# Kernel optimization log

Measured on AMD Instinct MI355X. Metric: run time of the kernel, lower is better.

The kernel has to match this reference:

```python
import jax, jax.numpy as jnp
import numpy as np

B, Tc, E, K, M, V = 8, 1024, 256, 8, 2048, 16
T1 = Tc * K          # penultimate layer length = 8192
TLAST = M * K        # last layer length = 16384


def setup_inputs() -> dict:
    key = jax.random.key(0)
    ks = jax.random.split(key, 12)
    x = jax.random.normal(ks[0], (B, Tc, E), jnp.float32)
    # penultimate values: exactly M 'mixed' tokens (value==2) per row, rest in {1,3}
    base = jnp.where(jnp.arange(T1) < M, 2, 1 + 2 * jax.random.randint(ks[1], (B, T1), 0, 2))
    perm = jnp.argsort(jax.random.uniform(ks[2], (B, T1)), axis=1)
    val1 = jnp.take_along_axis(base, perm, axis=1)
    vallast = 1 + 2 * jax.random.randint(ks[3], (B, TLAST), 0, 2)
    value = jnp.concatenate([val1, vallast], axis=1).astype(jnp.int64)
    depth = jnp.concatenate([jnp.full((B, T1), 5), jnp.full((B, TLAST), 6)], axis=1).astype(jnp.int64)
    pos = jax.random.randint(ks[4], (B, T1 + TLAST, 3), 0, 64).astype(jnp.int64)
    s = 0.02
    W1 = s * jax.random.normal(ks[5], (E, E, K), jnp.float32)  # ConvTranspose1d weight [in,out,k]
    b1 = s * jax.random.normal(ks[6], (E,), jnp.float32)
    W0 = s * jax.random.normal(ks[7], (E, E, K), jnp.float32)
    b0 = s * jax.random.normal(ks[8], (E,), jnp.float32)
    Wl = s * jax.random.normal(ks[9], (V + 1, E), jnp.float32)
    bl = s * jax.random.normal(ks[10], (V + 1,), jnp.float32)
    return {"x": x, "value": value, "depth": depth, "pos": pos, "num_mix": M,
            "W1": W1, "b1": b1, "W0": W0, "b0": b0, "Wl": Wl, "bl": bl}


def _deconv(x, W, b):
    # ConvTranspose1d with kernel=stride=K: each token expands to K tokens
    n, t, e = x.shape
    o = W.shape[1]
    y = jnp.einsum('nte,eoj->ntjo', x, W)  # [N,T,K,O]
    return y.reshape(n, t * W.shape[2], o) + b


def reference(x, value, depth, pos, num_mix, W1, b1, W0, b0, Wl, bl):
    n, tc, e = x.shape
    k = W1.shape[2]
    t1 = tc * k
    max_depth = jnp.max(depth)
    len_1 = jnp.sum(depth == max_depth - 1, axis=1)               # [N]
    tt = jnp.arange(t1)
    val_1 = jnp.where(tt[None, :] < len_1[:, None], value[:, :t1], 0)  # padded penultimate values
    mix_mask = val_1 == 2                                         # [N,T1]
    mix_1 = jnp.sum(mix_mask, axis=1)                             # [N]
    y_1 = _deconv(x, W1, b1)                                      # [N,T1,E]
    # stable pack: bring positions with value==2 to the front, keep order
    order = jnp.argsort(jnp.where(mix_mask, 0, 1), axis=1, stable=True)
    sel = order[:, :num_mix]                                      # [N,M]
    x_0 = jnp.take_along_axis(y_1, sel[:, :, None], axis=1)       # [N,M,E]
    valid = (jnp.arange(num_mix)[None, :] < mix_1[:, None]).astype(x_0.dtype)
    x_0 = x_0 * valid[:, :, None]                                 # zero-pad beyond per-row mix count
    y_0 = _deconv(x_0, W0, b0)                                    # [N,M*K,E]
    return y_0 @ Wl.T + bl                                        # [N,M*K,V+1]
```

## Files before the change

### kernel.cpp

```cpp
#include <hip/hip_runtime.h>

typedef __attribute__((ext_vector_type(8))) short bf16x8;
typedef __attribute__((ext_vector_type(4))) float f32x4;

#define BB 8
#define TC 1024
#define EE 256
#define KJ 8
#define MSEL 2048
#define V1 17
#define T1 8192
#define TTOT 24576
#define BI_TOT 16384
#define NCOLP 160
#define WSTRIDE 264

#define SCAL_OFF 0
#define SEL_OFF  1024
#define GRP_OFF  (SEL_OFF + 65536)
#define WFT_OFF  (GRP_OFF + 524288)
#define B2_OFF   (WFT_OFF + NCOLP*WSTRIDE*2)
#define BF0_OFF  (B2_OFF + 640)
#define WCT_OFF  (BF0_OFF + 128)

__device__ __forceinline__ unsigned short f2bf(float f) {
    union { float f; unsigned u; } x; x.f = f;
    unsigned r = x.u + 0x7fffu + ((x.u >> 16) & 1u);
    return (unsigned short)(r >> 16);
}
__device__ __forceinline__ float bf2f(unsigned short h) {
    union { unsigned u; float f; } x; x.u = ((unsigned)h) << 16;
    return x.f;
}

__device__ __forceinline__ float blockReduceSum256(float v) {
    #pragma unroll
    for (int d = 32; d; d >>= 1) v += __shfl_down(v, d, 64);
    __shared__ float sm[4];
    int lane = threadIdx.x & 63, wid = threadIdx.x >> 6;
    if (lane == 0) sm[wid] = v;
    __syncthreads();
    return sm[0] + sm[1] + sm[2] + sm[3];
}

__global__ __launch_bounds__(256) void k_maxdepth(const int* depth, int* scal) {
    int idx = blockIdx.x * 256 + threadIdx.x;
    int4 d = ((const int4*)depth)[idx];
    int v = max(max(d.x, d.y), max(d.z, d.w));
    #pragma unroll
    for (int dd = 32; dd; dd >>= 1) v = max(v, __shfl_down(v, dd, 64));
    __shared__ int sm[4];
    int lane = threadIdx.x & 63, wid = threadIdx.x >> 6;
    if (lane == 0) sm[wid] = v;
    __syncthreads();
    if (threadIdx.x == 0) atomicMax(&scal[0], max(max(sm[0], sm[1]), max(sm[2], sm[3])));
    if (blockIdx.x == 0 && threadIdx.x < 31) scal[1 + threadIdx.x] = 0;
}

__global__ __launch_bounds__(256) void k_len1(const int* depth, int* scal) {
    int idx = blockIdx.x * 256 + threadIdx.x;
    int b = blockIdx.x / 24;
    int md1 = scal[0] - 1;
    int4 d = ((const int4*)depth)[idx];
    int c = (d.x == md1) + (d.y == md1) + (d.z == md1) + (d.w == md1);
    #pragma unroll
    for (int dd = 32; dd; dd >>= 1) c += __shfl_down(c, dd, 64);
    __shared__ int sm[4];
    int lane = threadIdx.x & 63, wid = threadIdx.x >> 6;
    if (lane == 0) sm[wid] = c;
    __syncthreads();
    if (threadIdx.x == 0) {
        int t = sm[0] + sm[1] + sm[2] + sm[3];
        if (t) atomicAdd(&scal[1 + b], t);
    }
}

__global__ __launch_bounds__(256) void k_scan(const int* value, int* scal, int* sel) {
    int b = blockIdx.x, tid = threadIdx.x;
    int len1 = scal[1 + b];
    const int* vb = value + b * TTOT;
    int t0 = tid * 32;
    unsigned mask = 0;
    #pragma unroll
    for (int k = 0; k < 32; k += 4) {
        int4 v = *(const int4*)(vb + t0 + k);
        if (t0 + k + 0 < len1 && v.x == 2) mask |= 1u << (k + 0);
        if (t0 + k + 1 < len1 && v.y == 2) mask |= 1u << (k + 1);
        if (t0 + k + 2 < len1 && v.z == 2) mask |= 1u << (k + 2);
        if (t0 + k + 3 < len1 && v.w == 2) mask |= 1u << (k + 3);
    }
    int cnt = __popc(mask);
    int inc = cnt;
    #pragma unroll
    for (int d = 1; d < 64; d <<= 1) {
        int n = __shfl_up(inc, d, 64);
        if ((tid & 63) >= d) inc += n;
    }
    __shared__ int wt[4];
    int lane = tid & 63, wid = tid >> 6;
    if (lane == 63) wt[wid] = inc;
    __syncthreads();
    int woff = 0;
    for (int w = 0; w < wid; ++w) woff += wt[w];
    int off = woff + inc - cnt;
    #pragma unroll
    for (int k = 0; k < 32; ++k) {
        if (mask & (1u << k)) {
            if (off < MSEL) sel[b * MSEL + off] = t0 + k;
            off++;
        }
    }
    if (tid == 0) scal[9 + b] = wt[0] + wt[1] + wt[2] + wt[3];
}

__global__ __launch_bounds__(256) void k_wfused(const float* W0, const float* Wl, unsigned short* wfT) {
    int em = blockIdx.x;
    __shared__ float w0s[EE * KJ];
    __shared__ float wls[V1 * 257];
    for (int idx = threadIdx.x; idx < EE * KJ; idx += 256) w0s[idx] = W0[em * EE * KJ + idx];
    for (int idx = threadIdx.x; idx < V1 * EE; idx += 256) {
        int v = idx >> 8, o = idx & 255;
        wls[v * 257 + o] = Wl[idx];
    }
    __syncthreads();
    int tid = threadIdx.x;
    if (tid < 136) {
        int j = tid / V1, v = tid - j * V1;
        float acc = 0.f;
        #pragma unroll 4
        for (int o = 0; o < EE; ++o) acc += w0s[o * KJ + j] * wls[v * 257 + o];
        wfT[(j * 20 + v) * WSTRIDE + em] = f2bf(acc);
    }
}

__global__ __launch_bounds__(256) void k_grpbias(const int* sel, int* scal, int* groups,
        const float* b0, const float* bl, const float* b1, const float* Wl,
        const unsigned short* wfT, float* bias2, float* bf0) {
    int bid = blockIdx.x, tid = threadIdx.x;
    if (bid < 64) {
        __shared__ int lcnt[KJ], lbase[KJ];
        if (tid < KJ) lcnt[tid] = 0;
        __syncthreads();
        int idx = bid * 256 + tid;
        int b = idx >> 11;
        int valid = ((idx & (MSEL - 1)) < scal[9 + b]) ? 1 : 0;
        int t = valid ? sel[idx] : 0;
        int g = t & 7, tq = t >> 3;
        int lslot = atomicAdd(&lcnt[g], 1);
        __syncthreads();
        if (tid < KJ) lbase[tid] = atomicAdd(&scal[17 + tid], lcnt[tid]);
        __syncthreads();
        groups[g * BI_TOT + lbase[g] + lslot] = (idx << 11) | (tq << 1) | valid;
    } else if (bid < 81) {
        int v = bid - 64;
        float s = blockReduceSum256(b0[tid] * Wl[v * EE + tid]);
        if (tid == 0) bf0[v] = s + bl[v];
    } else {
        int c17 = bid - 81;
        int j = c17 / V1, v = c17 - j * V1;
        int colP = j * 20 + v;
        float s = blockReduceSum256(b1[tid] * bf2f(wfT[colP * WSTRIDE + tid]));
        if (tid == 0) bias2[colP] = s;
    }
}

__global__ __launch_bounds__(256) void k_wcomb(const float* W1, const unsigned short* wfT,
                                               unsigned short* wct) {
    int g = blockIdx.x >> 3;
    int e0 = (blockIdx.x & 7) * 32;
    __shared__ __align__(16) unsigned short b1s[32 * WSTRIDE];
    __shared__ __align__(16) unsigned short af[NCOLP * 72];
    int tid = threadIdx.x;
    {
        int em_l = tid & 63;
        int eb = (tid >> 6) * 8;
        #pragma unroll
        for (int i = 0; i < 8; ++i) {
            int e = eb + i;
            #pragma unroll
            for (int c = 0; c < 4; ++c) {
                int em = c * 64 + em_l;
                b1s[e * WSTRIDE + em] = f2bf(W1[(e0 + e) * (EE * KJ) + em * KJ + g]);
            }
        }
    }
    for (int idx = tid; idx < 1280; idx += 256) {
        int row = idx >> 3, f = idx & 7;
        ((int4*)af)[row * 9 + f] = ((const int4*)wfT)[row * 33 + f];
    }
    __syncthreads();

    int w = tid >> 6, l = tid & 63;
    int ntile = w & 1, mhalf = w >> 1;
    int lr = l & 15, lq = l >> 4;
    f32x4 acc[5];
    #pragma unroll
    for (int t = 0; t < 5; ++t) acc[t] = (f32x4){0.f, 0.f, 0.f, 0.f};

    for (int ch = 0; ch < 4; ++ch) {
        if (ch) {
            __syncthreads();
            for (int idx = tid; idx < 1280; idx += 256) {
                int row = idx >> 3, f = idx & 7;
                ((int4*)af)[row * 9 + f] = ((const int4*)wfT)[row * 33 + ch * 8 + f];
            }
            __syncthreads();
        }
        #pragma unroll
        for (int s = 0; s < 2; ++s) {
            bf16x8 bfr = *(const bf16x8*)&b1s[(ntile * 16 + lr) * WSTRIDE + ch * 64 + s * 32 + lq * 8];
            #pragma unroll
            for (int t = 0; t < 5; ++t) {
                bf16x8 afr = *(const bf16x8*)&af[((mhalf * 5 + t) * 16 + lr) * 72 + s * 32 + lq * 8];
                acc[t] = __builtin_amdgcn_mfma_f32_16x16x32_bf16(afr, bfr, acc[t], 0, 0, 0);
            }
        }
    }
    #pragma unroll
    for (int t = 0; t < 5; ++t) {
        int m = (mhalf * 5 + t) * 16 + lq * 4;
        int n = e0 + ntile * 16 + lr;
        #pragma unroll
        for (int r = 0; r < 4; ++r)
            wct[(g * NCOLP + m + r) * WSTRIDE + n] = f2bf(acc[t][r]);
    }
}

__global__ __launch_bounds__(256) void k_main(const float* x, const unsigned short* wct,
        const int* scal, const int* groups, const float* bias2, const float* bf0, float* out) {
    int g = blockIdx.x >> 9;
    int tile = blockIdx.x & 511;
    int cntg = scal[17 + g];
    if (tile * 32 >= cntg) return;
    int nrows = min(32, cntg - tile * 32);

    __shared__ __align__(16) unsigned short xs[32 * WSTRIDE];
    __shared__ __align__(16) unsigned short wts[NCOLP * 72];
    __shared__ int xoffs[32], obase[32];
    __shared__ unsigned char vflag[32];

    int tid = threadIdx.x;
    if (tid < 32) {
        int flag = 0, xo = 0, ob = 0;
        if (tid < nrows) {
            int p = groups[g * BI_TOT + tile * 32 + tid];
            int valid = p & 1;
            int tq = (p >> 1) & 1023;
            int bi = p >> 11;
            int b = bi >> 11;
            xo = (b * TC + tq) * EE;
            ob = bi * 136;
            flag = 1 + valid;
        }
        xoffs[tid] = xo; obase[tid] = ob; vflag[tid] = (unsigned char)flag;
    }
    __syncthreads();
    {
        int row = tid >> 3, q = tid & 7;
        const float* xp = x + xoffs[row];
        #pragma unroll
        for (int i = 0; i < 8; ++i) {
            int f4 = q + 8 * i;
            float4 v = *(const float4*)(xp + f4 * 4);
            ushort4 pk;
            pk.x = f2bf(v.x); pk.y = f2bf(v.y); pk.z = f2bf(v.z); pk.w = f2bf(v.w);
            *(ushort4*)&xs[row * WSTRIDE + f4 * 4] = pk;
        }
    }
    const int4* wsrc = (const int4*)wct;
    for (int idx = tid; idx < 1280; idx += 256) {
        int row = idx >> 3, f = idx & 7;
        ((int4*)wts)[row * 9 + f] = wsrc[(g * NCOLP + row) * 33 + f];
    }
    __syncthreads();

    int w = tid >> 6, l = tid & 63;
    int rw = w & 1, chalf = w >> 1;
    int lr = l & 15, lq = l >> 4;
    f32x4 acc[5];
    #pragma unroll
    for (int t = 0; t < 5; ++t) acc[t] = (f32x4){0.f, 0.f, 0.f, 0.f};

    for (int ch = 0; ch < 4; ++ch) {
        if (ch) {
            __syncthreads();
            for (int idx = tid; idx < 1280; idx += 256) {
                int row = idx >> 3, f = idx & 7;
                ((int4*)wts)[row * 9 + f] = wsrc[(g * NCOLP + row) * 33 + ch * 8 + f];
            }
            __syncthreads();
        }
        #pragma unroll
        for (int s = 0; s < 2; ++s) {
            bf16x8 afr = *(const bf16x8*)&xs[(rw * 16 + lr) * WSTRIDE + ch * 64 + s * 32 + lq * 8];
            #pragma unroll
            for (int t = 0; t < 5; ++t) {
                bf16x8 bfr = *(const bf16x8*)&wts[((chalf * 5 + t) * 16 + lr) * 72 + s * 32 + lq * 8];
                acc[t] = __builtin_amdgcn_mfma_f32_16x16x32_bf16(afr, bfr, acc[t], 0, 0, 0);
            }
        }
    }
    #pragma unroll
    for (int t = 0; t < 5; ++t) {
        int col = (chalf * 5 + t) * 16 + lr;
        int j = col / 20, v = col % 20;
        if (v < V1) {
            float bb = bias2[col] + bf0[v];
            float b0v = bf0[v];
            #pragma unroll
            for (int r = 0; r < 4; ++r) {
                int row = rw * 16 + lq * 4 + r;
                int fl = vflag[row];
                if (fl) out[obase[row] + j * V1 + v] = (fl == 2) ? (acc[t][r] + bb) : b0v;
            }
        }
    }
}

extern "C" void kernel_launch(void* const* d_in, const int* in_sizes, int n_in,
                              void* d_out, int out_size, void* d_ws, size_t ws_size,
                              hipStream_t stream) {
    const float* x     = (const float*)d_in[0];
    const int*   value = (const int*)d_in[1];
    const int*   depth = (const int*)d_in[2];
    const float* W1    = (const float*)d_in[5];
    const float* b1    = (const float*)d_in[6];
    const float* W0    = (const float*)d_in[7];
    const float* b0    = (const float*)d_in[8];
    const float* Wl    = (const float*)d_in[9];
    const float* bl    = (const float*)d_in[10];
    float* out = (float*)d_out;
    char* ws = (char*)d_ws;

    int*            scal   = (int*)(ws + SCAL_OFF);
    int*            sel    = (int*)(ws + SEL_OFF);
    int*            groups = (int*)(ws + GRP_OFF);
    unsigned short* wfT    = (unsigned short*)(ws + WFT_OFF);
    float*          bias2  = (float*)(ws + B2_OFF);
    float*          bf0    = (float*)(ws + BF0_OFF);
    unsigned short* wct    = (unsigned short*)(ws + WCT_OFF);

    k_maxdepth<<<dim3(192), dim3(256), 0, stream>>>(depth, scal);
    k_len1    <<<dim3(192), dim3(256), 0, stream>>>(depth, scal);
    k_scan    <<<dim3(BB),  dim3(256), 0, stream>>>(value, scal, sel);
    k_wfused  <<<dim3(EE),  dim3(256), 0, stream>>>(W0, Wl, wfT);
    k_grpbias <<<dim3(217), dim3(256), 0, stream>>>(sel, scal, groups, b0, bl, b1, Wl, wfT, bias2, bf0);
    k_wcomb   <<<dim3(64),  dim3(256), 0, stream>>>(W1, wfT, wct);
    k_main    <<<dim3(4096), dim3(256), 0, stream>>>(x, wct, scal, groups, bias2, bf0, out);
}
```

Before: 129.6 us.

## Fuse all seven kernels into one cooperative persistent kernel with grid syncs

Replaces the seven separate kernel launches with a single cooperative kernel of 256 blocks that runs three phases split by grid.sync. Phase one fuses the max-depth and length reductions with the W0·Wl weight fusion. Phase two builds the weight combination, scan and grouping, and bias terms. Phase three loops persistently over the output tiles. This removes launch gaps and the intermediate sel buffer, and padded rows are now written directly into group 0. The trade-offs are grid-barrier cost and a main phase limited to 256 persistent blocks, which may lower overlap compared with 4096 independent blocks.

```diff
diff --git a/kernel.cpp b/kernel.cpp
--- a/kernel.cpp
+++ b/kernel.cpp
@@ -1,4 +1,7 @@
 #include <hip/hip_runtime.h>
+#include <hip/hip_cooperative_groups.h>
+
+namespace cg = cooperative_groups;
 
 typedef __attribute__((ext_vector_type(8))) short bf16x8;
 typedef __attribute__((ext_vector_type(4))) float f32x4;
@@ -16,8 +19,7 @@
 #define WSTRIDE 264
 
 #define SCAL_OFF 0
-#define SEL_OFF  1024
-#define GRP_OFF  (SEL_OFF + 65536)
+#define GRP_OFF  1024
 #define WFT_OFF  (GRP_OFF + 524288)
 #define B2_OFF   (WFT_OFF + NCOLP*WSTRIDE*2)
 #define BF0_OFF  (B2_OFF + 640)
@@ -34,89 +36,28 @@
 }
 
 __device__ __forceinline__ float blockReduceSum256(float v) {
+    __shared__ float sm[4];
     #pragma unroll
     for (int d = 32; d; d >>= 1) v += __shfl_down(v, d, 64);
-    __shared__ float sm[4];
     int lane = threadIdx.x & 63, wid = threadIdx.x >> 6;
     if (lane == 0) sm[wid] = v;
     __syncthreads();
-    return sm[0] + sm[1] + sm[2] + sm[3];
-}
-
-__global__ __launch_bounds__(256) void k_maxdepth(const int* depth, int* scal) {
-    int idx = blockIdx.x * 256 + threadIdx.x;
-    int4 d = ((const int4*)depth)[idx];
-    int v = max(max(d.x, d.y), max(d.z, d.w));
-    #pragma unroll
-    for (int dd = 32; dd; dd >>= 1) v = max(v, __shfl_down(v, dd, 64));
-    __shared__ int sm[4];
-    int lane = threadIdx.x & 63, wid = threadIdx.x >> 6;
-    if (lane == 0) sm[wid] = v;
-    __syncthreads();
-    if (threadIdx.x == 0) atomicMax(&scal[0], max(max(sm[0], sm[1]), max(sm[2], sm[3])));
-    if (blockIdx.x == 0 && threadIdx.x < 31) scal[1 + threadIdx.x] = 0;
-}
-
-__global__ __launch_bounds__(256) void k_len1(const int* depth, int* scal) {
-    int idx = blockIdx.x * 256 + threadIdx.x;
-    int b = blockIdx.x / 24;
-    int md1 = scal[0] - 1;
-    int4 d = ((const int4*)depth)[idx];
-    int c = (d.x == md1) + (d.y == md1) + (d.z == md1) + (d.w == md1);
-    #pragma unroll
-    for (int dd = 32; dd; dd >>= 1) c += __shfl_down(c, dd, 64);
-    __shared__ int sm[4];
-    int lane = threadIdx.x & 63, wid = threadIdx.x >> 6;
-    if (lane == 0) sm[wid] = c;
-    __syncthreads();
-    if (threadIdx.x == 0) {
-        int t = sm[0] + sm[1] + sm[2] + sm[3];
-        if (t) atomicAdd(&scal[1 + b], t);
-    }
-}
-
-__global__ __launch_bounds__(256) void k_scan(const int* value, int* scal, int* sel) {
-    int b = blockIdx.x, tid = threadIdx.x;
-    int len1 = scal[1 + b];
-    const int* vb = value + b * TTOT;
-    int t0 = tid * 32;
-    unsigned mask = 0;
-    #pragma unroll
-    for (int k = 0; k < 32; k += 4) {
-        int4 v = *(const int4*)(vb + t0 + k);
-        if (t0 + k + 0 < len1 && v.x == 2) mask |= 1u << (k + 0);
-        if (t0 + k + 1 < len1 && v.y == 2) mask |= 1u << (k + 1);
-        if (t0 + k + 2 < len1 && v.z == 2) mask |= 1u << (k + 2);
-        if (t0 + k + 3 < len1 && v.w == 2) mask |= 1u << (k + 3);
-    }
-    int cnt = __popc(mask);
-    int inc = cnt;
-    #pragma unroll
-    for (int d = 1; d < 64; d <<= 1) {
-        int n = __shfl_up(inc, d, 64);
-        if ((tid & 63) >= d) inc += n;
-    }
-    __shared__ int wt[4];
-    int lane = tid & 63, wid = tid >> 6;
-    if (lane == 63) wt[wid] = inc;
-    __syncthreads();
-    int woff = 0;
-    for (int w = 0; w < wid; ++w) woff += wt[w];
-    int off = woff + inc - cnt;
-    #pragma unroll
-    for (int k = 0; k < 32; ++k) {
-        if (mask & (1u << k)) {
-            if (off < MSEL) sel[b * MSEL + off] = t0 + k;
-            off++;
-        }
-    }
-    if (tid == 0) scal[9 + b] = wt[0] + wt[1] + wt[2] + wt[3];
-}
-
-__global__ __launch_bounds__(256) void k_wfused(const float* W0, const float* Wl, unsigned short* wfT) {
-    int em = blockIdx.x;
-    __shared__ float w0s[EE * KJ];
-    __shared__ float wls[V1 * 257];
+    float r = sm[0] + sm[1] + sm[2] + sm[3];
+    __syncthreads();
+    return r;
+}
+
+union SMem {
+    struct { float w0s[EE * KJ]; float wls[V1 * 257]; } f;
+    struct { unsigned short b1s[32 * WSTRIDE]; unsigned short af[NCOLP * 72]; } w;
+    struct { unsigned short xs[32 * WSTRIDE]; unsigned short wts[NCOLP * 72];
+             int xoffs[32]; int obase[32]; unsigned char vflag[32]; } m;
+};
+
+__device__ void wfused_one(int em, const float* W0, const float* Wl, unsigned short* wfT, SMem& sm) {
+    __syncthreads();
+    float* w0s = sm.f.w0s;
+    float* wls = sm.f.wls;
     for (int idx = threadIdx.x; idx < EE * KJ; idx += 256) w0s[idx] = W0[em * EE * KJ + idx];
     for (int idx = threadIdx.x; idx < V1 * EE; idx += 256) {
         int v = idx >> 8, o = idx & 255;
@@ -133,117 +74,16 @@
     }
 }
 
-__global__ __launch_bounds__(256) void k_grpbias(const int* sel, int* scal, int* groups,
-        const float* b0, const float* bl, const float* b1, const float* Wl,
-        const unsigned short* wfT, float* bias2, float* bf0) {
-    int bid = blockIdx.x, tid = threadIdx.x;
-    if (bid < 64) {
-        __shared__ int lcnt[KJ], lbase[KJ];
-        if (tid < KJ) lcnt[tid] = 0;
-        __syncthreads();
-        int idx = bid * 256 + tid;
-        int b = idx >> 11;
-        int valid = ((idx & (MSEL - 1)) < scal[9 + b]) ? 1 : 0;
-        int t = valid ? sel[idx] : 0;
-        int g = t & 7, tq = t >> 3;
-        int lslot = atomicAdd(&lcnt[g], 1);
-        __syncthreads();
-        if (tid < KJ) lbase[tid] = atomicAdd(&scal[17 + tid], lcnt[tid]);
-        __syncthreads();
-        groups[g * BI_TOT + lbase[g] + lslot] = (idx << 11) | (tq << 1) | valid;
-    } else if (bid < 81) {
-        int v = bid - 64;
-        float s = blockReduceSum256(b0[tid] * Wl[v * EE + tid]);
-        if (tid == 0) bf0[v] = s + bl[v];
-    } else {
-        int c17 = bid - 81;
-        int j = c17 / V1, v = c17 - j * V1;
-        int colP = j * 20 + v;
-        float s = blockReduceSum256(b1[tid] * bf2f(wfT[colP * WSTRIDE + tid]));
-        if (tid == 0) bias2[colP] = s;
-    }
-}
-
-__global__ __launch_bounds__(256) void k_wcomb(const float* W1, const unsigned short* wfT,
-                                               unsigned short* wct) {
-    int g = blockIdx.x >> 3;
-    int e0 = (blockIdx.x & 7) * 32;
-    __shared__ __align__(16) unsigned short b1s[32 * WSTRIDE];
-    __shared__ __align__(16) unsigned short af[NCOLP * 72];
+__device__ void main_tile(int g, int t, int cntg, const float* x, const unsigned short* wct,
+                          const int* groups, const float* bias2, const float* bf0,
+                          float* out, SMem& sm) {
     int tid = threadIdx.x;
-    {
-        int em_l = tid & 63;
-        int eb = (tid >> 6) * 8;
-        #pragma unroll
-        for (int i = 0; i < 8; ++i) {
-            int e = eb + i;
-            #pragma unroll
-            for (int c = 0; c < 4; ++c) {
-                int em = c * 64 + em_l;
-                b1s[e * WSTRIDE + em] = f2bf(W1[(e0 + e) * (EE * KJ) + em * KJ + g]);
-            }
-        }
-    }
-    for (int idx = tid; idx < 1280; idx += 256) {
-        int row = idx >> 3, f = idx & 7;
-        ((int4*)af)[row * 9 + f] = ((const int4*)wfT)[row * 33 + f];
-    }
-    __syncthreads();
-
-    int w = tid >> 6, l = tid & 63;
-    int ntile = w & 1, mhalf = w >> 1;
-    int lr = l & 15, lq = l >> 4;
-    f32x4 acc[5];
-    #pragma unroll
-    for (int t = 0; t < 5; ++t) acc[t] = (f32x4){0.f, 0.f, 0.f, 0.f};
-
-    for (int ch = 0; ch < 4; ++ch) {
-        if (ch) {
-            __syncthreads();
-            for (int idx = tid; idx < 1280; idx += 256) {
-                int row = idx >> 3, f = idx & 7;
-                ((int4*)af)[row * 9 + f] = ((const int4*)wfT)[row * 33 + ch * 8 + f];
-            }
-            __syncthreads();
-        }
-        #pragma unroll
-        for (int s = 0; s < 2; ++s) {
-            bf16x8 bfr = *(const bf16x8*)&b1s[(ntile * 16 + lr) * WSTRIDE + ch * 64 + s * 32 + lq * 8];
-            #pragma unroll
-            for (int t = 0; t < 5; ++t) {
-                bf16x8 afr = *(const bf16x8*)&af[((mhalf * 5 + t) * 16 + lr) * 72 + s * 32 + lq * 8];
-                acc[t] = __builtin_amdgcn_mfma_f32_16x16x32_bf16(afr, bfr, acc[t], 0, 0, 0);
-            }
-        }
-    }
-    #pragma unroll
-    for (int t = 0; t < 5; ++t) {
-        int m = (mhalf * 5 + t) * 16 + lq * 4;
-        int n = e0 + ntile * 16 + lr;
-        #pragma unroll
-        for (int r = 0; r < 4; ++r)
-            wct[(g * NCOLP + m + r) * WSTRIDE + n] = f2bf(acc[t][r]);
-    }
-}
-
-__global__ __launch_bounds__(256) void k_main(const float* x, const unsigned short* wct,
-        const int* scal, const int* groups, const float* bias2, const float* bf0, float* out) {
-    int g = blockIdx.x >> 9;
-    int tile = blockIdx.x & 511;
-    int cntg = scal[17 + g];
-    if (tile * 32 >= cntg) return;
-    int nrows = min(32, cntg - tile * 32);
-
-    __shared__ __align__(16) unsigned short xs[32 * WSTRIDE];
-    __shared__ __align__(16) unsigned short wts[NCOLP * 72];
-    __shared__ int xoffs[32], obase[32];
-    __shared__ unsigned char vflag[32];
-
-    int tid = threadIdx.x;
+    int nrows = min(32, cntg - t * 32);
+    __syncthreads();
     if (tid < 32) {
         int flag = 0, xo = 0, ob = 0;
         if (tid < nrows) {
-            int p = groups[g * BI_TOT + tile * 32 + tid];
+            int p = groups[g * BI_TOT + t * 32 + tid];
             int valid = p & 1;
             int tq = (p >> 1) & 1023;
             int bi = p >> 11;
@@ -252,25 +92,25 @@
             ob = bi * 136;
             flag = 1 + valid;
         }
-        xoffs[tid] = xo; obase[tid] = ob; vflag[tid] = (unsigned char)flag;
+        sm.m.xoffs[tid] = xo; sm.m.obase[tid] = ob; sm.m.vflag[tid] = (unsigned char)flag;
     }
     __syncthreads();
     {
         int row = tid >> 3, q = tid & 7;
-        const float* xp = x + xoffs[row];
+        const float* xp = x + sm.m.xoffs[row];
         #pragma unroll
         for (int i = 0; i < 8; ++i) {
             int f4 = q + 8 * i;
             float4 v = *(const float4*)(xp + f4 * 4);
             ushort4 pk;
             pk.x = f2bf(v.x); pk.y = f2bf(v.y); pk.z = f2bf(v.z); pk.w = f2bf(v.w);
-            *(ushort4*)&xs[row * WSTRIDE + f4 * 4] = pk;
+            *(ushort4*)&sm.m.xs[row * WSTRIDE + f4 * 4] = pk;
         }
     }
     const int4* wsrc = (const int4*)wct;
     for (int idx = tid; idx < 1280; idx += 256) {
         int row = idx >> 3, f = idx & 7;
-        ((int4*)wts)[row * 9 + f] = wsrc[(g * NCOLP + row) * 33 + f];
+        ((int4*)sm.m.wts)[row * 9 + f] = wsrc[(g * NCOLP + row) * 33 + f];
     }
     __syncthreads();
 
@@ -279,30 +119,30 @@
     int lr = l & 15, lq = l >> 4;
     f32x4 acc[5];
     #pragma unroll
-    for (int t = 0; t < 5; ++t) acc[t] = (f32x4){0.f, 0.f, 0.f, 0.f};
+    for (int tt = 0; tt < 5; ++tt) acc[tt] = (f32x4){0.f, 0.f, 0.f, 0.f};
 
     for (int ch = 0; ch < 4; ++ch) {
         if (ch) {
             __syncthreads();
             for (int idx = tid; idx < 1280; idx += 256) {
                 int row = idx >> 3, f = idx & 7;
-                ((int4*)wts)[row * 9 + f] = wsrc[(g * NCOLP + row) * 33 + ch * 8 + f];
+                ((int4*)sm.m.wts)[row * 9 + f] = wsrc[(g * NCOLP + row) * 33 + ch * 8 + f];
             }
             __syncthreads();
         }
         #pragma unroll
         for (int s = 0; s < 2; ++s) {
-            bf16x8 afr = *(const bf16x8*)&xs[(rw * 16 + lr) * WSTRIDE + ch * 64 + s * 32 + lq * 8];
-            #pragma unroll
-            for (int t = 0; t < 5; ++t) {
-                bf16x8 bfr = *(const bf16x8*)&wts[((chalf * 5 + t) * 16 + lr) * 72 + s * 32 + lq * 8];
-                acc[t] = __builtin_amdgcn_mfma_f32_16x16x32_bf16(afr, bfr, acc[t], 0, 0, 0);
+            bf16x8 afr = *(const bf16x8*)&sm.m.xs[(rw * 16 + lr) * WSTRIDE + ch * 64 + s * 32 + lq * 8];
+            #pragma unroll
+            for (int tt = 0; tt < 5; ++tt) {
+                bf16x8 bfr = *(const bf16x8*)&sm.m.wts[((chalf * 5 + tt) * 16 + lr) * 72 + s * 32 + lq * 8];
+                acc[tt] = __builtin_amdgcn_mfma_f32_16x16x32_bf16(afr, bfr, acc[tt], 0, 0, 0);
             }
         }
     }
     #pragma unroll
-    for (int t = 0; t < 5; ++t) {
-        int col = (chalf * 5 + t) * 16 + lr;
+    for (int tt = 0; tt < 5; ++tt) {
+        int col = (chalf * 5 + tt) * 16 + lr;
         int j = col / 20, v = col % 20;
         if (v < V1) {
             float bb = bias2[col] + bf0[v];
@@ -310,10 +150,215 @@
             #pragma unroll
             for (int r = 0; r < 4; ++r) {
                 int row = rw * 16 + lq * 4 + r;
-                int fl = vflag[row];
-                if (fl) out[obase[row] + j * V1 + v] = (fl == 2) ? (acc[t][r] + bb) : b0v;
-            }
-        }
+                int fl = sm.m.vflag[row];
+                if (fl) out[sm.m.obase[row] + j * V1 + v] = (fl == 2) ? (acc[tt][r] + bb) : b0v;
+            }
+        }
+    }
+}
+
+__global__ __launch_bounds__(256) void k_all(
+        const float* x, const int* value, const int* depth,
+        const float* W1, const float* b1, const float* W0, const float* b0,
+        const float* Wl, const float* bl, float* out,
+        int* scal, int* groups, unsigned short* wfT, float* bias2, float* bf0,
+        unsigned short* wct) {
+    __shared__ SMem sm;
+    __shared__ int s_red[4];
+    __shared__ int s_wt[4], s_lcnt[8], s_lcnt2[8], s_lbase[8];
+    cg::grid_group grid = cg::this_grid();
+    int bid = blockIdx.x, tid = threadIdx.x;
+
+    if (bid == 0 && tid < 8) scal[33 + tid] = 0;
+    if (bid < 248) {
+        wfused_one(bid, W0, Wl, wfT, sm);
+        if (bid < 8) wfused_one(248 + bid, W0, Wl, wfT, sm);
+    } else {
+        int b = bid - 248;
+        const int4* dp = (const int4*)(depth + b * TTOT);
+        int m = -2147483648;
+        for (int i = tid; i < 6144; i += 256) {
+            int4 d = dp[i];
+            m = max(max(m, max(d.x, d.y)), max(d.z, d.w));
+        }
+        #pragma unroll
+        for (int dd = 32; dd; dd >>= 1) m = max(m, __shfl_down(m, dd, 64));
+        if ((tid & 63) == 0) s_red[tid >> 6] = m;
+        __syncthreads();
+        int bmax = max(max(s_red[0], s_red[1]), max(s_red[2], s_red[3]));
+        if (tid == 0) { atomicMax(&scal[0], bmax); scal[1 + b] = bmax; }
+        int c1 = 0, c2 = 0;
+        for (int i = tid; i < 6144; i += 256) {
+            int4 d = dp[i];
+            c1 += (d.x == bmax) + (d.y == bmax) + (d.z == bmax) + (d.w == bmax);
+            c2 += (d.x == bmax - 1) + (d.y == bmax - 1) + (d.z == bmax - 1) + (d.w == bmax - 1);
+        }
+        int cc = (c1 << 16) + c2;
+        #pragma unroll
+        for (int dd = 32; dd; dd >>= 1) cc += __shfl_down(cc, dd, 64);
+        __syncthreads();
+        if ((tid & 63) == 0) s_red[tid >> 6] = cc;
+        __syncthreads();
+        if (tid == 0) {
+            int tot = s_red[0] + s_red[1] + s_red[2] + s_red[3];
+            scal[9 + b] = tot >> 16;
+            scal[17 + b] = tot & 0xffff;
+        }
+    }
+    grid.sync();
+
+    if (bid < 64) {
+        int g = bid >> 3;
+        int e0 = (bid & 7) * 32;
+        unsigned short* b1s = sm.w.b1s;
+        unsigned short* af = sm.w.af;
+        {
+            int em_l = tid & 63;
+            int eb = (tid >> 6) * 8;
+            #pragma unroll
+            for (int i = 0; i < 8; ++i) {
+                int e = eb + i;
+                #pragma unroll
+                for (int c = 0; c < 4; ++c) {
+                    int em = c * 64 + em_l;
+                    b1s[e * WSTRIDE + em] = f2bf(W1[(e0 + e) * (EE * KJ) + em * KJ + g]);
+                }
+            }
+        }
+        for (int idx = tid; idx < 1280; idx += 256) {
+            int row = idx >> 3, f = idx & 7;
+            ((int4*)af)[row * 9 + f] = ((const int4*)wfT)[row * 33 + f];
+        }
+        __syncthreads();
+
+        int w = tid >> 6, l = tid & 63;
+        int ntile = w & 1, mhalf = w >> 1;
+        int lr = l & 15, lq = l >> 4;
+        f32x4 acc[5];
+        #pragma unroll
+        for (int t = 0; t < 5; ++t) acc[t] = (f32x4){0.f, 0.f, 0.f, 0.f};
+
+        for (int ch = 0; ch < 4; ++ch) {
+            if (ch) {
+                __syncthreads();
+                for (int idx = tid; idx < 1280; idx += 256) {
+                    int row = idx >> 3, f = idx & 7;
+                    ((int4*)af)[row * 9 + f] = ((const int4*)wfT)[row * 33 + ch * 8 + f];
+                }
+                __syncthreads();
+            }
+            #pragma unroll
+            for (int s = 0; s < 2; ++s) {
+                bf16x8 bfr = *(const bf16x8*)&b1s[(ntile * 16 + lr) * WSTRIDE + ch * 64 + s * 32 + lq * 8];
+                #pragma unroll
+                for (int t = 0; t < 5; ++t) {
+                    bf16x8 afr = *(const bf16x8*)&af[((mhalf * 5 + t) * 16 + lr) * 72 + s * 32 + lq * 8];
+                    acc[t] = __builtin_amdgcn_mfma_f32_16x16x32_bf16(afr, bfr, acc[t], 0, 0, 0);
+                }
+            }
+        }
+        #pragma unroll
+        for (int t = 0; t < 5; ++t) {
+            int m = (mhalf * 5 + t) * 16 + lq * 4;
+            int n = e0 + ntile * 16 + lr;
+            #pragma unroll
+            for (int r = 0; r < 4; ++r)
+                wct[(g * NCOLP + m + r) * WSTRIDE + n] = f2bf(acc[t][r]);
+        }
+    } else if (bid < 72) {
+        int b = bid - 64;
+        int gmax = scal[0];
+        int mb = scal[1 + b], cm = scal[9 + b], cm1 = scal[17 + b];
+        int len1 = (mb == gmax) ? cm1 : ((mb == gmax - 1) ? cm : 0);
+        const int* vb = value + b * TTOT;
+        int t0 = tid * 32;
+        unsigned mask = 0;
+        #pragma unroll
+        for (int k = 0; k < 32; k += 4) {
+            int4 v = *(const int4*)(vb + t0 + k);
+            if (t0 + k + 0 < len1 && v.x == 2) mask |= 1u << (k + 0);
+            if (t0 + k + 1 < len1 && v.y == 2) mask |= 1u << (k + 1);
+            if (t0 + k + 2 < len1 && v.z == 2) mask |= 1u << (k + 2);
+            if (t0 + k + 3 < len1 && v.w == 2) mask |= 1u << (k + 3);
+        }
+        int cnt = __popc(mask);
+        int inc = cnt;
+        #pragma unroll
+        for (int d = 1; d < 64; d <<= 1) {
+            int n = __shfl_up(inc, d, 64);
+            if ((tid & 63) >= d) inc += n;
+        }
+        int lane = tid & 63, wid = tid >> 6;
+        if (lane == 63) s_wt[wid] = inc;
+        if (tid < 8) { s_lcnt[tid] = 0; s_lcnt2[tid] = 0; }
+        __syncthreads();
+        int woff = 0;
+        for (int w = 0; w < wid; ++w) woff += s_wt[w];
+        int off0 = woff + inc - cnt;
+        int mix1 = s_wt[0] + s_wt[1] + s_wt[2] + s_wt[3];
+        int mix1c = min(mix1, MSEL);
+        {
+            int off = off0;
+            #pragma unroll
+            for (int k = 0; k < 32; ++k) {
+                if (mask & (1u << k)) {
+                    if (off < MSEL) atomicAdd(&s_lcnt[(t0 + k) & 7], 1);
+                    off++;
+                }
+            }
+        }
+        if (tid == 0 && mix1c < MSEL) atomicAdd(&s_lcnt[0], MSEL - mix1c);
+        __syncthreads();
+        if (tid < 8) s_lbase[tid] = atomicAdd(&scal[33 + tid], s_lcnt[tid]);
+        __syncthreads();
+        {
+            int off = off0;
+            #pragma unroll
+            for (int k = 0; k < 32; ++k) {
+                if (mask & (1u << k)) {
+                    if (off < MSEL) {
+                        int t = t0 + k;
+                        int g = t & 7;
+                        int ls = atomicAdd(&s_lcnt2[g], 1);
+                        groups[g * BI_TOT + s_lbase[g] + ls] =
+                            ((b * MSEL + off) << 11) | ((t >> 3) << 1) | 1;
+                    }
+                    off++;
+                }
+            }
+        }
+        for (int i = mix1c + tid; i < MSEL; i += 256) {
+            int ls = atomicAdd(&s_lcnt2[0], 1);
+            groups[s_lbase[0] + ls] = (b * MSEL + i) << 11;
+        }
+    } else if (bid < 89) {
+        int v = bid - 72;
+        float s = blockReduceSum256(b0[tid] * Wl[v * EE + tid]);
+        if (tid == 0) bf0[v] = s + bl[v];
+    } else if (bid < 157) {
+        #pragma unroll
+        for (int r = 0; r < 2; ++r) {
+            int c17 = (bid - 89) * 2 + r;
+            int j = c17 / V1, v = c17 - j * V1;
+            int colP = j * 20 + v;
+            float s = blockReduceSum256(b1[tid] * bf2f(wfT[colP * WSTRIDE + tid]));
+            if (tid == 0) bias2[colP] = s;
+        }
+    }
+    grid.sync();
+
+    int cntv[8], tb[9];
+    tb[0] = 0;
+    #pragma unroll
+    for (int g = 0; g < 8; ++g) {
+        cntv[g] = scal[33 + g];
+        tb[g + 1] = tb[g] + ((cntv[g] + 31) >> 5);
+    }
+    int total = tb[8];
+    for (int T = bid; T < total; T += 256) {
+        int g = 0;
+        while (T >= tb[g + 1]) ++g;
+        main_tile(g, T - tb[g], cntv[g], x, wct, groups, bias2, bf0, out, sm);
     }
 }
 
@@ -333,18 +378,13 @@
     char* ws = (char*)d_ws;
 
     int*            scal   = (int*)(ws + SCAL_OFF);
-    int*            sel    = (int*)(ws + SEL_OFF);
     int*            groups = (int*)(ws + GRP_OFF);
     unsigned short* wfT    = (unsigned short*)(ws + WFT_OFF);
     float*          bias2  = (float*)(ws + B2_OFF);
     float*          bf0    = (float*)(ws + BF0_OFF);
     unsigned short* wct    = (unsigned short*)(ws + WCT_OFF);
 
-    k_maxdepth<<<dim3(192), dim3(256), 0, stream>>>(depth, scal);
-    k_len1    <<<dim3(192), dim3(256), 0, stream>>>(depth, scal);
-    k_scan    <<<dim3(BB),  dim3(256), 0, stream>>>(value, scal, sel);
-    k_wfused  <<<dim3(EE),  dim3(256), 0, stream>>>(W0, Wl, wfT);
-    k_grpbias <<<dim3(217), dim3(256), 0, stream>>>(sel, scal, groups, b0, bl, b1, Wl, wfT, bias2, bf0);
-    k_wcomb   <<<dim3(64),  dim3(256), 0, stream>>>(W1, wfT, wct);
-    k_main    <<<dim3(4096), dim3(256), 0, stream>>>(x, wct, scal, groups, bias2, bf0, out);
-}
+    void* args[] = { &x, &value, &depth, &W1, &b1, &W0, &b0, &Wl, &bl, &out,
+                     &scal, &groups, &wfT, &bias2, &bf0, &wct };
+    hipLaunchCooperativeKernel((void*)k_all, dim3(256), dim3(256), args, 0, stream);
+}
```

New measurement: 219.6 us. +69.5%, slower.
